# Kernel tuning notes

Measured on AMD Instinct MI355X. Metric: run time of the kernel, lower is better.

Reference implementation:

```python
import jax, jax.numpy as jnp
import numpy as np
import math

BASE = 10000
N_HEADS = 16


def _rope_cos_sin(seq_len, head_dim, dtype=jnp.float32):
    # thetas = base ** (-2 * (arange(hd//2) / hd))
    thetas = BASE ** (-2.0 * (jnp.arange(head_dim // 2, dtype=jnp.float32) / head_dim))
    freqs = jnp.arange(seq_len, dtype=jnp.float32)[:, None] * thetas[None, :]  # [S, hd/2]
    return jnp.cos(freqs).astype(dtype), jnp.sin(freqs).astype(dtype)


def _apply_rope(x, cos, sin):
    # x: [B, H, S, D]; complex multiply on consecutive (even, odd) pairs
    b, h, s, d = x.shape
    xr = x.reshape(b, h, s, d // 2, 2)
    x0, x1 = xr[..., 0], xr[..., 1]
    c = cos[None, None, :, :]
    sn = sin[None, None, :, :]
    o0 = x0 * c - x1 * sn
    o1 = x0 * sn + x1 * c
    return jnp.stack([o0, o1], axis=-1).reshape(b, h, s, d)


def setup_inputs() -> dict:
    key = jax.random.key(0)
    k1, k2, k3 = jax.random.split(key, 3)
    B, S, E = 2, 2048, 1024
    x = jax.random.normal(k1, (B, S, E), dtype=jnp.float32)
    W_qkv = jax.random.normal(k2, (3 * E, E), dtype=jnp.float32) * (1.0 / math.sqrt(E))
    W_o = jax.random.normal(k3, (E, E), dtype=jnp.float32) * (1.0 / math.sqrt(E))
    return {"x": x, "W_qkv": W_qkv, "W_o": W_o}


def reference(x, W_qkv, W_o):
    B, S, E = x.shape
    H = N_HEADS
    D = E // H
    qkv = x @ W_qkv.T  # [B, S, 3E]
    q, k, v = jnp.split(qkv, 3, axis=-1)
    # [B, S, E] -> [B, H, S, D]
    q = q.reshape(B, S, H, D).transpose(0, 2, 1, 3)
    k = k.reshape(B, S, H, D).transpose(0, 2, 1, 3)
    v = v.reshape(B, S, H, D).transpose(0, 2, 1, 3)
    cos, sin = _rope_cos_sin(S, D)
    q = _apply_rope(q, cos, sin)
    k = _apply_rope(k, cos, sin)
    scores = jnp.einsum("bhqd,bhkd->bhqk", q, k) / math.sqrt(D)
    causal = jnp.tril(jnp.ones((S, S), dtype=bool))
    scores = jnp.where(causal[None, None, :, :], scores, -jnp.inf)
    wts = jax.nn.softmax(scores, axis=-1)
    y = jnp.einsum("bhqk,bhkd->bhqd", wts, v)
    y = y.transpose(0, 2, 1, 3).reshape(B, S, E)
    return y @ W_o.T
```

## Files before the change

kernel.cpp:

```cpp
#include <hip/hip_runtime.h>
#include <math.h>
#include <stdint.h>

typedef __bf16 bf16;
typedef __bf16 bf16x4 __attribute__((ext_vector_type(4)));
typedef __bf16 bf16x8 __attribute__((ext_vector_type(8)));
typedef float  f32x4  __attribute__((ext_vector_type(4)));

#define QSCALE 0.18033688011112042f

#define XB_OFF    ((size_t)0)
#define WQKV_OFF  ((size_t)8388608)
#define WO_OFF    ((size_t)14680064)
#define QB_OFF    ((size_t)16777216)
#define KB_OFF    ((size_t)25165824)
#define VB_OFF    ((size_t)33554432)
#define YB_OFF    ((size_t)41943040)
#define COS_OFF   ((size_t)50331648)
#define SIN_OFF   ((size_t)50593792)

__device__ __forceinline__ void gload_lds16(const void* g, void* l) {
  __builtin_amdgcn_global_load_lds((const __attribute__((address_space(1))) void*)g,
                                   (__attribute__((address_space(3))) void*)l,
                                   16, 0, 0);
}

__global__ void cvt_f32_bf16(const float* __restrict__ src, bf16* __restrict__ dst, int n4) {
  int i = blockIdx.x * blockDim.x + threadIdx.x;
  if (i >= n4) return;
  float4 v = ((const float4*)src)[i];
  bf16x4 o = {(bf16)v.x, (bf16)v.y, (bf16)v.z, (bf16)v.w};
  *(bf16x4*)(dst + (size_t)i * 4) = o;
}

__global__ void rope_table(float* __restrict__ cosT, float* __restrict__ sinT) {
  int i = blockIdx.x * blockDim.x + threadIdx.x;
  int s = i >> 5, f = i & 31;
  float theta = exp2f(-(float)f * (13.287712379549449f / 32.0f));
  float ang = (float)s * theta;
  cosT[i] = cosf(ang);
  sinT[i] = sinf(ang);
}

__global__ __launch_bounds__(256) void transpose_v(const bf16* __restrict__ Vb,
                                                   bf16* __restrict__ Vt) {
  __shared__ bf16 t[64][72];
  const int st = blockIdx.x, bh = blockIdx.y;
  const size_t head = (size_t)bh * 2048 * 64;
  const bf16* src = Vb + head + (size_t)st * 64 * 64;
#pragma unroll
  for (int c = 0; c < 2; ++c) {
    int idx = c * 256 + threadIdx.x;
    int row = idx >> 3, col = (idx & 7) << 3;
    bf16x8 v = *(const bf16x8*)&src[row * 64 + col];
#pragma unroll
    for (int j = 0; j < 8; ++j) t[col + j][row] = v[j];
  }
  __syncthreads();
  bf16* dst = Vt + head + (size_t)st * 64;
#pragma unroll
  for (int c = 0; c < 2; ++c) {
    int idx = c * 256 + threadIdx.x;
    int d = idx >> 3, s8 = (idx & 7) << 3;
    *(bf16x8*)&dst[(size_t)d * 2048 + s8] = *(const bf16x8*)&t[d][s8];
  }
}

template <int EPI, int NJ>
__global__ __launch_bounds__(256) void gemm_nt(
    const bf16* __restrict__ A, const bf16* __restrict__ Bw, float* __restrict__ Cout,
    bf16* __restrict__ Qb, bf16* __restrict__ Kb, bf16* __restrict__ Vb,
    const float* __restrict__ cosT, const float* __restrict__ sinT,
    int M, int N, int K)
{
  constexpr int BN  = NJ * 32;
  constexpr int ASZ = 128 * 64;
  constexpr int BSZ = BN * 64;
  __shared__ bf16 smem[ASZ + BSZ];
  bf16* sA = smem;
  bf16* sB = smem + ASZ;

  const int tid  = threadIdx.x;
  const int w    = tid >> 6;
  const int lane = tid & 63;
  const int quad = lane >> 4;
  const int l16  = lane & 15;
  const int wm   = (w >> 1) * 64;
  const int wn   = (w & 1) * (NJ * 16);
  const int tm   = blockIdx.y * 128;
  const int tn   = blockIdx.x * BN;
  const int srow = lane >> 3;
  const int scol = ((lane & 7) ^ srow) << 3;
  const int rsw  = l16 & 7;

  f32x4 zero4 = {0.f, 0.f, 0.f, 0.f};
  f32x4 acc[4][NJ];
#pragma unroll
  for (int i = 0; i < 4; ++i)
#pragma unroll
    for (int j = 0; j < NJ; ++j) acc[i][j] = zero4;

  const bf16* Abase = A + (size_t)tm * K;
  const bf16* Bbase = Bw + (size_t)tn * K;

  for (int k0 = 0; k0 < K; k0 += 64) {
#pragma unroll
    for (int c = 0; c < 4; ++c) {
      const int rb = (w * 4 + c) * 8;
      gload_lds16(Abase + (size_t)(rb + srow) * K + (k0 + scol), &sA[rb * 64]);
    }
#pragma unroll
    for (int c = 0; c < BN / 32; ++c) {
      const int rb = (w * (BN / 32) + c) * 8;
      gload_lds16(Bbase + (size_t)(rb + srow) * K + (k0 + scol), &sB[rb * 64]);
    }
    __syncthreads();
#pragma unroll
    for (int kk = 0; kk < 2; ++kk) {
      bf16x8 af[4], bfr[NJ];
#pragma unroll
      for (int i = 0; i < 4; ++i)
        af[i] = *(const bf16x8*)&sA[(wm + i * 16 + l16) * 64 + (((kk * 4 + quad) ^ rsw) << 3)];
#pragma unroll
      for (int j = 0; j < NJ; ++j)
        bfr[j] = *(const bf16x8*)&sB[(wn + j * 16 + l16) * 64 + (((kk * 4 + quad) ^ rsw) << 3)];
#pragma unroll
      for (int i = 0; i < 4; ++i)
#pragma unroll
        for (int j = 0; j < NJ; ++j)
          acc[i][j] = __builtin_amdgcn_mfma_f32_16x16x32_bf16(af[i], bfr[j], acc[i][j], 0, 0, 0);
    }
    __syncthreads();
  }

  if constexpr (EPI == 0) {
#pragma unroll
    for (int i = 0; i < 4; ++i) {
      const int rowb = wm + i * 16 + quad * 4;
#pragma unroll
      for (int j = 0; j < 4; ++j) {
        const int col = wn + j * 16 + l16;
        const int ch = col >> 3, cl = col & 7;
#pragma unroll
        for (int r = 0; r < 4; ++r) {
          const int row = rowb + r;
          const int key = (row >> 2) & 7;
          const int ph = (ch & 8) | ((ch ^ key) & 7);
          smem[row * 128 + ph * 8 + cl] = (bf16)acc[i][j][r];
        }
      }
    }
    __syncthreads();
    const int row  = tid >> 1;
    const int half = tid & 1;
    const int m = tm + row;
    const int b = m >> 11, s = m & 2047;
    const int nbase = tn + half * 64;
    const int g = nbase >> 10;
    const int h = (nbase & 1023) >> 6;
    bf16* dst = (g == 2) ? Vb : ((g == 0) ? Qb : Kb);
    const size_t obase = ((size_t)((b << 4) + h) * 2048 + s) * 64;
    const int key = (row >> 2) & 7;
#pragma unroll
    for (int c = 0; c < 8; ++c) {
      const int ch = half * 8 + c;
      const int ph = (ch & 8) | ((ch ^ key) & 7);
      bf16x8 v = *(const bf16x8*)&smem[row * 128 + ph * 8];
      if (g == 2) {
        *(bf16x8*)&dst[obase + c * 8] = v;
      } else {
        f32x4 c4 = *(const f32x4*)&cosT[s * 32 + c * 4];
        f32x4 s4 = *(const f32x4*)&sinT[s * 32 + c * 4];
        bf16x8 ov;
#pragma unroll
        for (int t = 0; t < 4; ++t) {
          float x0 = (float)v[2 * t], x1 = (float)v[2 * t + 1];
          float o0 = x0 * c4[t] - x1 * s4[t];
          float o1 = x0 * s4[t] + x1 * c4[t];
          if (g == 0) { o0 *= QSCALE; o1 *= QSCALE; }
          ov[2 * t] = (bf16)o0;
          ov[2 * t + 1] = (bf16)o1;
        }
        *(bf16x8*)&dst[obase + c * 8] = ov;
      }
    }
  } else {
#pragma unroll
    for (int i = 0; i < 4; ++i)
#pragma unroll
      for (int j = 0; j < NJ; ++j)
#pragma unroll
        for (int r = 0; r < 4; ++r) {
          const int m = tm + wm + i * 16 + quad * 4 + r;
          const int n = tn + wn + j * 16 + l16;
          Cout[(size_t)m * N + n] = acc[i][j][r];
        }
  }
}

__global__ __launch_bounds__(256) void attn_fwd(
    const bf16* __restrict__ Qb, const bf16* __restrict__ Kb,
    const bf16* __restrict__ Vt, bf16* __restrict__ Yb)
{
  __shared__ bf16 sK[2][64 * 64];
  __shared__ bf16 sV[2][64 * 64];
  __shared__ bf16 sP[64 * 68];

  const int bh  = blockIdx.x;
  const int p   = blockIdx.y;
  const int tid = threadIdx.x;
  const int w    = tid >> 6;
  const int lane = tid & 63;
  const int quad = lane >> 4;
  const int l16  = lane & 15;

  const size_t head = (size_t)bh * 2048 * 64;
  const bf16* khead = Kb + head;
  const bf16* vhead = Vt + head;

  const int srow = lane >> 3;
  const int scol = ((lane & 7) ^ srow) << 3;
  const int rs   = l16 & 7;
  const int cb0  = (quad ^ rs) << 3;
  const int cb1  = ((quad + 4) ^ rs) << 3;

  f32x4 zero4 = {0.f, 0.f, 0.f, 0.f};
  const int b = bh >> 4, h = bh & 15;
  const int prow = (w * 16 + l16) * 68;

  auto stage = [&](int kt, int bsel) {
    const bf16* ks = khead + (size_t)kt * 4096;
    const bf16* vs = vhead + kt * 64;
#pragma unroll
    for (int c = 0; c < 2; ++c) {
      const int chunk = (w << 1) + c;
      const int row = (chunk << 3) + srow;
      gload_lds16(ks + row * 64 + scol,           &sK[bsel][chunk * 512]);
      gload_lds16(vs + (size_t)row * 2048 + scol, &sV[bsel][chunk * 512]);
    }
  };

  for (int pass = 0; pass < 2; ++pass) {
    const int qt = pass ? (31 - p) : p;
    const int nk = qt + 1;

    const bf16* qsrc = Qb + head + (size_t)qt * 4096;
    bf16x8 bq0 = *(const bf16x8*)&qsrc[(w * 16 + l16) * 64 + quad * 8];
    bf16x8 bq1 = *(const bf16x8*)&qsrc[(w * 16 + l16) * 64 + 32 + quad * 8];

    f32x4 o[4] = {zero4, zero4, zero4, zero4};
    float mi = -3.0e38f;
    float li = 0.f;
    const int qpos = qt * 64 + w * 16 + l16;

    __syncthreads();
    stage(0, 0);

    for (int kt = 0; kt < nk; ++kt) {
      __syncthreads();
      if (kt + 1 < nk) stage(kt + 1, (kt + 1) & 1);

      const bf16* bK = sK[kt & 1];
      const bf16* bV = sV[kt & 1];

      f32x4 sv[4];
#pragma unroll
      for (int i = 0; i < 4; ++i) {
        const int m = i * 16 + l16;
        bf16x8 k0 = *(const bf16x8*)&bK[m * 64 + cb0];
        bf16x8 k1 = *(const bf16x8*)&bK[m * 64 + cb1];
        f32x4 cacc = zero4;
        cacc = __builtin_amdgcn_mfma_f32_16x16x32_bf16(k0, bq0, cacc, 0, 0, 0);
        cacc = __builtin_amdgcn_mfma_f32_16x16x32_bf16(k1, bq1, cacc, 0, 0, 0);
        sv[i] = cacc;
      }

      if (kt == qt) {
#pragma unroll
        for (int i = 0; i < 4; ++i) {
          int kbase = kt * 64 + i * 16 + quad * 4;
#pragma unroll
          for (int r = 0; r < 4; ++r)
            sv[i][r] = (kbase + r > qpos) ? -3.0e38f : sv[i][r];
        }
      }

      float mx = sv[0][0];
#pragma unroll
      for (int i = 0; i < 4; ++i)
#pragma unroll
        for (int r = 0; r < 4; ++r) mx = fmaxf(mx, sv[i][r]);
      mx = fmaxf(mx, __shfl_xor(mx, 16));
      mx = fmaxf(mx, __shfl_xor(mx, 32));
      float mn = fmaxf(mi, mx);
      float al = exp2f(mi - mn);
      float pv[4][4];
      float rsum = 0.f;
#pragma unroll
      for (int i = 0; i < 4; ++i)
#pragma unroll
        for (int r = 0; r < 4; ++r) {
          float pe = exp2f(sv[i][r] - mn);
          pv[i][r] = pe;
          rsum += pe;
        }
      rsum += __shfl_xor(rsum, 16);
      rsum += __shfl_xor(rsum, 32);
      li = li * al + rsum;
      mi = mn;

      float af[4];
#pragma unroll
      for (int r = 0; r < 4; ++r) af[r] = __shfl(al, quad * 4 + r);
#pragma unroll
      for (int i = 0; i < 4; ++i)
#pragma unroll
        for (int r = 0; r < 4; ++r) o[i][r] *= af[r];

#pragma unroll
      for (int i = 0; i < 4; ++i) {
        bf16x4 pk = {(bf16)pv[i][0], (bf16)pv[i][1], (bf16)pv[i][2], (bf16)pv[i][3]};
        *(bf16x4*)&sP[prow + i * 16 + quad * 4] = pk;
      }
      bf16x8 ap0 = *(const bf16x8*)&sP[prow + quad * 8];
      bf16x8 ap1 = *(const bf16x8*)&sP[prow + 32 + quad * 8];
#pragma unroll
      for (int i = 0; i < 4; ++i) {
        const int m = i * 16 + l16;
        bf16x8 v0 = *(const bf16x8*)&bV[m * 64 + cb0];
        bf16x8 v1 = *(const bf16x8*)&bV[m * 64 + cb1];
        o[i] = __builtin_amdgcn_mfma_f32_16x16x32_bf16(ap0, v0, o[i], 0, 0, 0);
        o[i] = __builtin_amdgcn_mfma_f32_16x16x32_bf16(ap1, v1, o[i], 0, 0, 0);
      }
    }

#pragma unroll
    for (int r = 0; r < 4; ++r) {
      float inv = 1.0f / __shfl(li, quad * 4 + r);
      int s = qt * 64 + w * 16 + quad * 4 + r;
      size_t base = ((size_t)(b * 2048 + s)) * 1024 + h * 64;
#pragma unroll
      for (int i = 0; i < 4; ++i)
        Yb[base + i * 16 + l16] = (bf16)(o[i][r] * inv);
    }
  }
}

extern "C" void kernel_launch(void* const* d_in, const int* in_sizes, int n_in,
                              void* d_out, int out_size, void* d_ws, size_t ws_size,
                              hipStream_t stream) {
  (void)in_sizes; (void)n_in; (void)out_size; (void)ws_size;
  const float* x    = (const float*)d_in[0];
  const float* wqkv = (const float*)d_in[1];
  const float* wo   = (const float*)d_in[2];
  float* out = (float*)d_out;
  char* ws = (char*)d_ws;

  bf16* Xb    = (bf16*)(ws + XB_OFF);
  bf16* Wqkvb = (bf16*)(ws + WQKV_OFF);
  bf16* Wob   = (bf16*)(ws + WO_OFF);
  bf16* Qb    = (bf16*)(ws + QB_OFF);
  bf16* Kb    = (bf16*)(ws + KB_OFF);
  bf16* Vb    = (bf16*)(ws + VB_OFF);
  bf16* Vtb   = (bf16*)(ws + XB_OFF);
  bf16* Yb    = (bf16*)(ws + YB_OFF);
  float* cosT = (float*)(ws + COS_OFF);
  float* sinT = (float*)(ws + SIN_OFF);

  rope_table<<<(2048 * 32) / 256, 256, 0, stream>>>(cosT, sinT);
  cvt_f32_bf16<<<4096, 256, 0, stream>>>(x,    Xb,    (4096 * 1024) / 4);
  cvt_f32_bf16<<<3072, 256, 0, stream>>>(wqkv, Wqkvb, (3072 * 1024) / 4);
  cvt_f32_bf16<<<1024, 256, 0, stream>>>(wo,   Wob,   (1024 * 1024) / 4);

  gemm_nt<0, 4><<<dim3(24, 32), 256, 0, stream>>>(Xb, Wqkvb, nullptr, Qb, Kb, Vb,
                                                  cosT, sinT, 4096, 3072, 1024);
  transpose_v<<<dim3(32, 32), 256, 0, stream>>>(Vb, Vtb);
  attn_fwd<<<dim3(32, 16), 256, 0, stream>>>(Qb, Kb, Vtb, Yb);
  gemm_nt<1, 2><<<dim3(16, 32), 256, 0, stream>>>(Yb, Wob, out, nullptr, nullptr, nullptr,
                                                  nullptr, nullptr, 4096, 1024, 1024);
}
```

Baseline: 203.0 us.

## Split attention into one q-tile per block, fuse conversions, swizzle P buffer

Merges the three fp32-to-bf16 conversion launches into a single kernel. The attention kernel now processes one query tile per block over a 32x32 grid, with tiles ordered by bit-reversal, instead of pairing tiles p and 31-p inside one block. This adds parallelism but loses the explicit balancing of causal work. It also switches the P staging buffer to an XOR-swizzled layout without padding to avoid LDS bank conflicts, and skips rescaling the output accumulator when the running max is unchanged across the wave.

```diff
diff --git a/kernel.cpp b/kernel.cpp
--- a/kernel.cpp
+++ b/kernel.cpp
@@ -25,12 +25,17 @@
                                    16, 0, 0);
 }
 
-__global__ void cvt_f32_bf16(const float* __restrict__ src, bf16* __restrict__ dst, int n4) {
+__global__ void cvt_all(const float* __restrict__ x, const float* __restrict__ wqkv,
+                        const float* __restrict__ wo, bf16* __restrict__ Xb,
+                        bf16* __restrict__ Wqkvb, bf16* __restrict__ Wob) {
   int i = blockIdx.x * blockDim.x + threadIdx.x;
-  if (i >= n4) return;
-  float4 v = ((const float4*)src)[i];
+  const float* src; bf16* dst; int off;
+  if (i < 1048576)      { src = x;    dst = Xb;    off = i; }
+  else if (i < 1835008) { src = wqkv; dst = Wqkvb; off = i - 1048576; }
+  else                  { src = wo;   dst = Wob;   off = i - 1835008; }
+  float4 v = ((const float4*)src)[off];
   bf16x4 o = {(bf16)v.x, (bf16)v.y, (bf16)v.z, (bf16)v.w};
-  *(bf16x4*)(dst + (size_t)i * 4) = o;
+  *(bf16x4*)(dst + (size_t)off * 4) = o;
 }
 
 __global__ void rope_table(float* __restrict__ cosT, float* __restrict__ sinT) {
@@ -204,10 +209,12 @@
 {
   __shared__ bf16 sK[2][64 * 64];
   __shared__ bf16 sV[2][64 * 64];
-  __shared__ bf16 sP[64 * 68];
+  __shared__ bf16 sP[64 * 64];
 
   const int bh  = blockIdx.x;
-  const int p   = blockIdx.y;
+  const int y   = blockIdx.y;
+  const int qt  = ((y & 1) << 4) | ((y & 2) << 2) | (y & 4) | ((y & 8) >> 2) | ((y & 16) >> 4);
+  const int nk  = qt + 1;
   const int tid = threadIdx.x;
   const int w    = tid >> 6;
   const int lane = tid & 63;
@@ -226,7 +233,7 @@
 
   f32x4 zero4 = {0.f, 0.f, 0.f, 0.f};
   const int b = bh >> 4, h = bh & 15;
-  const int prow = (w * 16 + l16) * 68;
+  const int prow = (w * 16 + l16) * 64;
 
   auto stage = [&](int kt, int bsel) {
     const bf16* ks = khead + (size_t)kt * 4096;
@@ -240,109 +247,106 @@
     }
   };
 
-  for (int pass = 0; pass < 2; ++pass) {
-    const int qt = pass ? (31 - p) : p;
-    const int nk = qt + 1;
-
-    const bf16* qsrc = Qb + head + (size_t)qt * 4096;
-    bf16x8 bq0 = *(const bf16x8*)&qsrc[(w * 16 + l16) * 64 + quad * 8];
-    bf16x8 bq1 = *(const bf16x8*)&qsrc[(w * 16 + l16) * 64 + 32 + quad * 8];
-
-    f32x4 o[4] = {zero4, zero4, zero4, zero4};
-    float mi = -3.0e38f;
-    float li = 0.f;
-    const int qpos = qt * 64 + w * 16 + l16;
-
+  const bf16* qsrc = Qb + head + (size_t)qt * 4096;
+  bf16x8 bq0 = *(const bf16x8*)&qsrc[(w * 16 + l16) * 64 + quad * 8];
+  bf16x8 bq1 = *(const bf16x8*)&qsrc[(w * 16 + l16) * 64 + 32 + quad * 8];
+
+  f32x4 o[4] = {zero4, zero4, zero4, zero4};
+  float mi = -3.0e38f;
+  float li = 0.f;
+  const int qpos = qt * 64 + w * 16 + l16;
+
+  stage(0, 0);
+
+  for (int kt = 0; kt < nk; ++kt) {
     __syncthreads();
-    stage(0, 0);
-
-    for (int kt = 0; kt < nk; ++kt) {
-      __syncthreads();
-      if (kt + 1 < nk) stage(kt + 1, (kt + 1) & 1);
-
-      const bf16* bK = sK[kt & 1];
-      const bf16* bV = sV[kt & 1];
-
-      f32x4 sv[4];
+    if (kt + 1 < nk) stage(kt + 1, (kt + 1) & 1);
+
+    const bf16* bK = sK[kt & 1];
+    const bf16* bV = sV[kt & 1];
+
+    f32x4 sv[4];
+#pragma unroll
+    for (int i = 0; i < 4; ++i) {
+      const int m = i * 16 + l16;
+      bf16x8 k0 = *(const bf16x8*)&bK[m * 64 + cb0];
+      bf16x8 k1 = *(const bf16x8*)&bK[m * 64 + cb1];
+      f32x4 cacc = zero4;
+      cacc = __builtin_amdgcn_mfma_f32_16x16x32_bf16(k0, bq0, cacc, 0, 0, 0);
+      cacc = __builtin_amdgcn_mfma_f32_16x16x32_bf16(k1, bq1, cacc, 0, 0, 0);
+      sv[i] = cacc;
+    }
+
+    if (kt == qt) {
 #pragma unroll
       for (int i = 0; i < 4; ++i) {
-        const int m = i * 16 + l16;
-        bf16x8 k0 = *(const bf16x8*)&bK[m * 64 + cb0];
-        bf16x8 k1 = *(const bf16x8*)&bK[m * 64 + cb1];
-        f32x4 cacc = zero4;
-        cacc = __builtin_amdgcn_mfma_f32_16x16x32_bf16(k0, bq0, cacc, 0, 0, 0);
-        cacc = __builtin_amdgcn_mfma_f32_16x16x32_bf16(k1, bq1, cacc, 0, 0, 0);
-        sv[i] = cacc;
+        int kbase = kt * 64 + i * 16 + quad * 4;
+#pragma unroll
+        for (int r = 0; r < 4; ++r)
+          sv[i][r] = (kbase + r > qpos) ? -3.0e38f : sv[i][r];
       }
-
-      if (kt == qt) {
-#pragma unroll
-        for (int i = 0; i < 4; ++i) {
-          int kbase = kt * 64 + i * 16 + quad * 4;
-#pragma unroll
-          for (int r = 0; r < 4; ++r)
-            sv[i][r] = (kbase + r > qpos) ? -3.0e38f : sv[i][r];
-        }
+    }
+
+    float mx = sv[0][0];
+#pragma unroll
+    for (int i = 0; i < 4; ++i)
+#pragma unroll
+      for (int r = 0; r < 4; ++r) mx = fmaxf(mx, sv[i][r]);
+    mx = fmaxf(mx, __shfl_xor(mx, 16));
+    mx = fmaxf(mx, __shfl_xor(mx, 32));
+    float mn = fmaxf(mi, mx);
+    float al = exp2f(mi - mn);
+    float pv[4][4];
+    float rsum = 0.f;
+#pragma unroll
+    for (int i = 0; i < 4; ++i)
+#pragma unroll
+      for (int r = 0; r < 4; ++r) {
+        float pe = exp2f(sv[i][r] - mn);
+        pv[i][r] = pe;
+        rsum += pe;
       }
-
-      float mx = sv[0][0];
+    rsum += __shfl_xor(rsum, 16);
+    rsum += __shfl_xor(rsum, 32);
+    li = li * al + rsum;
+
+    if (__any(mn > mi)) {
+      float af[4];
+#pragma unroll
+      for (int r = 0; r < 4; ++r) af[r] = __shfl(al, quad * 4 + r);
 #pragma unroll
       for (int i = 0; i < 4; ++i)
 #pragma unroll
-        for (int r = 0; r < 4; ++r) mx = fmaxf(mx, sv[i][r]);
-      mx = fmaxf(mx, __shfl_xor(mx, 16));
-      mx = fmaxf(mx, __shfl_xor(mx, 32));
-      float mn = fmaxf(mi, mx);
-      float al = exp2f(mi - mn);
-      float pv[4][4];
-      float rsum = 0.f;
-#pragma unroll
-      for (int i = 0; i < 4; ++i)
-#pragma unroll
-        for (int r = 0; r < 4; ++r) {
-          float pe = exp2f(sv[i][r] - mn);
-          pv[i][r] = pe;
-          rsum += pe;
-        }
-      rsum += __shfl_xor(rsum, 16);
-      rsum += __shfl_xor(rsum, 32);
-      li = li * al + rsum;
-      mi = mn;
-
-      float af[4];
-#pragma unroll
-      for (int r = 0; r < 4; ++r) af[r] = __shfl(al, quad * 4 + r);
-#pragma unroll
-      for (int i = 0; i < 4; ++i)
-#pragma unroll
         for (int r = 0; r < 4; ++r) o[i][r] *= af[r];
-
-#pragma unroll
-      for (int i = 0; i < 4; ++i) {
-        bf16x4 pk = {(bf16)pv[i][0], (bf16)pv[i][1], (bf16)pv[i][2], (bf16)pv[i][3]};
-        *(bf16x4*)&sP[prow + i * 16 + quad * 4] = pk;
-      }
-      bf16x8 ap0 = *(const bf16x8*)&sP[prow + quad * 8];
-      bf16x8 ap1 = *(const bf16x8*)&sP[prow + 32 + quad * 8];
-#pragma unroll
-      for (int i = 0; i < 4; ++i) {
-        const int m = i * 16 + l16;
-        bf16x8 v0 = *(const bf16x8*)&bV[m * 64 + cb0];
-        bf16x8 v1 = *(const bf16x8*)&bV[m * 64 + cb1];
-        o[i] = __builtin_amdgcn_mfma_f32_16x16x32_bf16(ap0, v0, o[i], 0, 0, 0);
-        o[i] = __builtin_amdgcn_mfma_f32_16x16x32_bf16(ap1, v1, o[i], 0, 0, 0);
-      }
-    }
-
-#pragma unroll
-    for (int r = 0; r < 4; ++r) {
-      float inv = 1.0f / __shfl(li, quad * 4 + r);
-      int s = qt * 64 + w * 16 + quad * 4 + r;
-      size_t base = ((size_t)(b * 2048 + s)) * 1024 + h * 64;
-#pragma unroll
-      for (int i = 0; i < 4; ++i)
-        Yb[base + i * 16 + l16] = (bf16)(o[i][r] * inv);
-    }
+    }
+    mi = mn;
+
+#pragma unroll
+    for (int i = 0; i < 4; ++i) {
+      bf16x4 pk = {(bf16)pv[i][0], (bf16)pv[i][1], (bf16)pv[i][2], (bf16)pv[i][3]};
+      const int ch = i * 2 + (quad >> 1);
+      *(bf16x4*)&sP[prow + ((ch ^ rs) << 3) + ((quad & 1) << 2)] = pk;
+    }
+    bf16x8 ap0 = *(const bf16x8*)&sP[prow + cb0];
+    bf16x8 ap1 = *(const bf16x8*)&sP[prow + cb1];
+#pragma unroll
+    for (int i = 0; i < 4; ++i) {
+      const int m = i * 16 + l16;
+      bf16x8 v0 = *(const bf16x8*)&bV[m * 64 + cb0];
+      bf16x8 v1 = *(const bf16x8*)&bV[m * 64 + cb1];
+      o[i] = __builtin_amdgcn_mfma_f32_16x16x32_bf16(ap0, v0, o[i], 0, 0, 0);
+      o[i] = __builtin_amdgcn_mfma_f32_16x16x32_bf16(ap1, v1, o[i], 0, 0, 0);
+    }
+  }
+
+#pragma unroll
+  for (int r = 0; r < 4; ++r) {
+    float inv = 1.0f / __shfl(li, quad * 4 + r);
+    int s = qt * 64 + w * 16 + quad * 4 + r;
+    size_t base = ((size_t)(b * 2048 + s)) * 1024 + h * 64;
+#pragma unroll
+    for (int i = 0; i < 4; ++i)
+      Yb[base + i * 16 + l16] = (bf16)(o[i][r] * inv);
   }
 }
 
@@ -368,14 +372,12 @@
   float* sinT = (float*)(ws + SIN_OFF);
 
   rope_table<<<(2048 * 32) / 256, 256, 0, stream>>>(cosT, sinT);
-  cvt_f32_bf16<<<4096, 256, 0, stream>>>(x,    Xb,    (4096 * 1024) / 4);
-  cvt_f32_bf16<<<3072, 256, 0, stream>>>(wqkv, Wqkvb, (3072 * 1024) / 4);
-  cvt_f32_bf16<<<1024, 256, 0, stream>>>(wo,   Wob,   (1024 * 1024) / 4);
+  cvt_all<<<8192, 256, 0, stream>>>(x, wqkv, wo, Xb, Wqkvb, Wob);
 
   gemm_nt<0, 4><<<dim3(24, 32), 256, 0, stream>>>(Xb, Wqkvb, nullptr, Qb, Kb, Vb,
                                                   cosT, sinT, 4096, 3072, 1024);
   transpose_v<<<dim3(32, 32), 256, 0, stream>>>(Vb, Vtb);
-  attn_fwd<<<dim3(32, 16), 256, 0, stream>>>(Qb, Kb, Vtb, Yb);
+  attn_fwd<<<dim3(32, 32), 256, 0, stream>>>(Qb, Kb, Vtb, Yb);
   gemm_nt<1, 2><<<dim3(16, 32), 256, 0, stream>>>(Yb, Wob, out, nullptr, nullptr, nullptr,
                                                   nullptr, nullptr, 4096, 1024, 1024);
 }
```

New measurement: 220.1 us. 8.4% more time.
